# Kernel tuning notes

Hardware: AMD Instinct MI355X
Metric: run time of the kernel (lower is better)

Reference implementation:

```python
import jax, jax.numpy as jnp
import numpy as np

H = 64  # hidden_size, hard-coded in module


def _lstm_layer(xs, W_ih, W_hh, b_ih, b_hh):
    """Run one LSTM layer over time-major xs [T, B, D_in].
    PyTorch gate order: i, f, g, o. Returns (hs [T,B,H], h_last [B,H])."""
    T, B, _ = xs.shape
    b = b_ih + b_hh
    # Precompute input contribution for all timesteps: [T, B, 4H]
    x_gates = jnp.einsum('tbd,gd->tbg', xs, W_ih) + b

    def step(carry, xg_t):
        h, c = carry
        gates = xg_t + h @ W_hh.T  # [B, 4H]
        i, f, g, o = jnp.split(gates, 4, axis=-1)
        i = jax.nn.sigmoid(i)
        f = jax.nn.sigmoid(f)
        g = jnp.tanh(g)
        o = jax.nn.sigmoid(o)
        c = f * c + i * g
        h = o * jnp.tanh(c)
        return (h, c), h

    h0 = jnp.zeros((B, H), xs.dtype)
    c0 = jnp.zeros((B, H), xs.dtype)
    (h_last, _), hs = jax.lax.scan(step, (h0, c0), x_gates)
    return hs, h_last


def setup_inputs() -> dict:
    key = jax.random.key(0)
    ks = jax.random.split(key, 12)
    B, T, C_in, E = 256, 4000, 1, 128
    s0 = 1.0 / np.sqrt(H)  # PyTorch LSTM init scale
    inp = {
        'x': jax.random.normal(ks[0], (B, T, C_in), jnp.float32),
        'W_ih0': jax.random.uniform(ks[1], (4 * H, C_in), jnp.float32, -s0, s0),
        'W_hh0': jax.random.uniform(ks[2], (4 * H, H), jnp.float32, -s0, s0),
        'b_ih0': jax.random.uniform(ks[3], (4 * H,), jnp.float32, -s0, s0),
        'b_hh0': jax.random.uniform(ks[4], (4 * H,), jnp.float32, -s0, s0),
        'W_ih1': jax.random.uniform(ks[5], (4 * H, H), jnp.float32, -s0, s0),
        'W_hh1': jax.random.uniform(ks[6], (4 * H, H), jnp.float32, -s0, s0),
        'b_ih1': jax.random.uniform(ks[7], (4 * H,), jnp.float32, -s0, s0),
        'b_hh1': jax.random.uniform(ks[8], (4 * H,), jnp.float32, -s0, s0),
        'W_fc': jax.random.uniform(ks[9], (E, H), jnp.float32, -s0, s0),
        'b_fc': jax.random.uniform(ks[10], (E,), jnp.float32, -s0, s0),
    }
    return inp


def reference(x, W_ih0, W_hh0, b_ih0, b_hh0, W_ih1, W_hh1, b_ih1, b_hh1, W_fc, b_fc):
    # x: [B, T, 1] (batch_first) -> time-major [T, B, 1]
    xs = jnp.swapaxes(x.astype(jnp.float32), 0, 1)
    hs0, _ = _lstm_layer(xs, W_ih0, W_hh0, b_ih0, b_hh0)
    _, h_last = _lstm_layer(hs0, W_ih1, W_hh1, b_ih1, b_hh1)
    # fc on final hidden state of the last layer: [B, E]
    return h_last @ W_fc.T + b_fc
```

## Files before the change

kernel.cpp:

```cpp
#include <hip/hip_runtime.h>

#define TT 4000
#define HH 64
#define NB 256
#define EE 128

typedef __attribute__((ext_vector_type(2))) _Float16 h2;
typedef __attribute__((ext_vector_type(8))) _Float16 h8;

__device__ __forceinline__ float ftanh(float x) {
    return fmaf(2.f, __builtin_amdgcn_rcpf(1.f + __expf(-2.f * x)), -1.f);
}

#if __has_builtin(__builtin_amdgcn_fdot2)
#define FDOT2(a, b, c) __builtin_amdgcn_fdot2((a), (b), (c), false)
#else
#define FDOT2(a, b, c) fmaf((float)(a).x, (float)(b).x, fmaf((float)(a).y, (float)(b).y, (c)))
#endif

#define H2V(V, i) (__builtin_shufflevector((V), (V), 2 * (i), 2 * (i) + 1))

template <int CTRL>
__device__ __forceinline__ float dpp_mov(float v) {
    return __int_as_float(__builtin_amdgcn_update_dpp(
        0, __float_as_int(v), CTRL, 0xF, 0xF, true));
}
#define DPP_XOR1 0xB1
#define DPP_XOR2 0x4E
#define DPP_FB   0x44
#define DPP_OB   0xEE
#define DPP_SHR4 0x114

#define CVT2(d0, d1, s) h2 d0 = h2{(_Float16)(s).x, (_Float16)(s).y}, \
                           d1 = h2{(_Float16)(s).z, (_Float16)(s).w};

__global__ __launch_bounds__(512, 2)
void lstm2_fc_kernel(const float* __restrict__ x,
                     const float* __restrict__ W_ih0,
                     const float* __restrict__ W_hh0,
                     const float* __restrict__ b_ih0,
                     const float* __restrict__ b_hh0,
                     const float* __restrict__ W_ih1,
                     const float* __restrict__ W_hh1,
                     const float* __restrict__ b_ih1,
                     const float* __restrict__ b_hh1,
                     const float* __restrict__ W_fc,
                     const float* __restrict__ b_fc,
                     float* __restrict__ out)
{
    const int b    = blockIdx.x;
    const int tid  = threadIdx.x;
    const int w    = tid >> 6;
    const int lane = tid & 63;
    const int ss   = lane & 1;
    const int uu   = (lane >> 1) & 1;
    const int pp   = (lane >> 2) & 1;
    const int nn   = (lane >> 3) & 1;
    const int n    = w * 8 + (lane >> 4) * 2 + nn;
    const int gidx = pp + 2 * uu;

    __shared__ float x_s[TT];
    __shared__ __align__(16) _Float16 hbuf[2][2 * HH];

    for (int t = tid; t < TT; t += 512) x_s[t] = x[(size_t)b * TT + t];
    if (tid < 4 * HH) ((_Float16*)hbuf)[tid] = (_Float16)0.f;

    const int row = gidx * HH + n;
    const float4* p0 = (const float4*)(W_hh0 + row * HH + ss * 32);
    const float4* p1 = (const float4*)(W_ih1 + row * HH + ss * 32);
    const float4* p2 = (const float4*)(W_hh1 + row * HH + ss * 32);
    float4 a0 = p0[0], a1 = p0[1], a2 = p0[2], a3 = p0[3];
    float4 a4 = p0[4], a5 = p0[5], a6 = p0[6], a7 = p0[7];
    float4 e0 = p1[0], e1 = p1[1], e2 = p1[2], e3 = p1[3];
    float4 e4 = p1[4], e5 = p1[5], e6 = p1[6], e7 = p1[7];
    float4 d0 = p2[0], d1 = p2[1], d2 = p2[2], d3 = p2[3];
    float4 d4 = p2[4], d5 = p2[5], d6 = p2[6], d7 = p2[7];
    CVT2(A0,  A1,  a0) CVT2(A2,  A3,  a1) CVT2(A4,  A5,  a2) CVT2(A6,  A7,  a3)
    CVT2(A8,  A9,  a4) CVT2(A10, A11, a5) CVT2(A12, A13, a6) CVT2(A14, A15, a7)
    CVT2(B0,  B1,  e0) CVT2(B2,  B3,  e1) CVT2(B4,  B5,  e2) CVT2(B6,  B7,  e3)
    CVT2(B8,  B9,  e4) CVT2(B10, B11, e5) CVT2(B12, B13, e6) CVT2(B14, B15, e7)
    CVT2(C0,  C1,  d0) CVT2(C2,  C3,  d1) CVT2(C4,  C5,  d2) CVT2(C6,  C7,  d3)
    CVT2(C8,  C9,  d4) CVT2(C10, C11, d5) CVT2(C12, C13, d6) CVT2(C14, C15, d7)

    float wx  = W_ih0[row];
    float bb0 = b_ih0[row] + b_hh0[row];
    float bb1 = b_ih1[row] + b_hh1[row];

    asm volatile("" : "+v"(A0), "+v"(A1), "+v"(A2),  "+v"(A3),
                      "+v"(A4), "+v"(A5), "+v"(A6),  "+v"(A7),
                      "+v"(A8), "+v"(A9), "+v"(A10), "+v"(A11),
                      "+v"(A12),"+v"(A13),"+v"(A14), "+v"(A15),
                      "+v"(B0), "+v"(B1), "+v"(B2),  "+v"(B3),
                      "+v"(B4), "+v"(B5), "+v"(B6),  "+v"(B7));
    asm volatile("" : "+v"(B8), "+v"(B9), "+v"(B10), "+v"(B11),
                      "+v"(B12),"+v"(B13),"+v"(B14), "+v"(B15),
                      "+v"(C0), "+v"(C1), "+v"(C2),  "+v"(C3),
                      "+v"(C4), "+v"(C5), "+v"(C6),  "+v"(C7),
                      "+v"(C8), "+v"(C9), "+v"(C10), "+v"(C11),
                      "+v"(C12),"+v"(C13),"+v"(C14), "+v"(C15),
                      "+v"(wx), "+v"(bb0),"+v"(bb1));

    const bool isg = (gidx == 2);
    const float kk = isg ? -2.f : -1.f;
    const float mm = isg ?  2.f :  1.f;
    const float aa = isg ? -1.f :  0.f;

    const bool wlane = (pp == 1) && (uu == 0);
    const int  hoff  = ss * HH + n;
    float cc = 0.f;

    __syncthreads();

    for (int t = 0; t <= TT; ++t) {
        const float xt = x_s[(t < TT) ? t : 0];
        const h8* hb = (const h8*)hbuf[t & 1];
        h8 Ha = hb[4 * ss + 0], Hc = hb[4 * ss + 1];
        h8 He = hb[4 * ss + 2], Hg = hb[4 * ss + 3];
        h8 Ga = hb[8 + 4 * ss + 0], Gc = hb[8 + 4 * ss + 1];
        h8 Ge = hb[8 + 4 * ss + 2], Gg = hb[8 + 4 * ss + 3];

        float acc0 = ss ? 0.f : fmaf(xt, wx, bb0);
        float acc1 = ss ? 0.f : bb1;
        acc0 = FDOT2(A0,  H2V(Ha, 0), acc0); acc0 = FDOT2(A1,  H2V(Ha, 1), acc0);
        acc0 = FDOT2(A2,  H2V(Ha, 2), acc0); acc0 = FDOT2(A3,  H2V(Ha, 3), acc0);
        acc0 = FDOT2(A4,  H2V(Hc, 0), acc0); acc0 = FDOT2(A5,  H2V(Hc, 1), acc0);
        acc0 = FDOT2(A6,  H2V(Hc, 2), acc0); acc0 = FDOT2(A7,  H2V(Hc, 3), acc0);
        acc0 = FDOT2(A8,  H2V(He, 0), acc0); acc0 = FDOT2(A9,  H2V(He, 1), acc0);
        acc0 = FDOT2(A10, H2V(He, 2), acc0); acc0 = FDOT2(A11, H2V(He, 3), acc0);
        acc0 = FDOT2(A12, H2V(Hg, 0), acc0); acc0 = FDOT2(A13, H2V(Hg, 1), acc0);
        acc0 = FDOT2(A14, H2V(Hg, 2), acc0); acc0 = FDOT2(A15, H2V(Hg, 3), acc0);

        acc1 = FDOT2(B0,  H2V(Ha, 0), acc1); acc1 = FDOT2(B1,  H2V(Ha, 1), acc1);
        acc1 = FDOT2(B2,  H2V(Ha, 2), acc1); acc1 = FDOT2(B3,  H2V(Ha, 3), acc1);
        acc1 = FDOT2(B4,  H2V(Hc, 0), acc1); acc1 = FDOT2(B5,  H2V(Hc, 1), acc1);
        acc1 = FDOT2(B6,  H2V(Hc, 2), acc1); acc1 = FDOT2(B7,  H2V(Hc, 3), acc1);
        acc1 = FDOT2(B8,  H2V(He, 0), acc1); acc1 = FDOT2(B9,  H2V(He, 1), acc1);
        acc1 = FDOT2(B10, H2V(He, 2), acc1); acc1 = FDOT2(B11, H2V(He, 3), acc1);
        acc1 = FDOT2(B12, H2V(Hg, 0), acc1); acc1 = FDOT2(B13, H2V(Hg, 1), acc1);
        acc1 = FDOT2(B14, H2V(Hg, 2), acc1); acc1 = FDOT2(B15, H2V(Hg, 3), acc1);
        acc1 = FDOT2(C0,  H2V(Ga, 0), acc1); acc1 = FDOT2(C1,  H2V(Ga, 1), acc1);
        acc1 = FDOT2(C2,  H2V(Ga, 2), acc1); acc1 = FDOT2(C3,  H2V(Ga, 3), acc1);
        acc1 = FDOT2(C4,  H2V(Gc, 0), acc1); acc1 = FDOT2(C5,  H2V(Gc, 1), acc1);
        acc1 = FDOT2(C6,  H2V(Gc, 2), acc1); acc1 = FDOT2(C7,  H2V(Gc, 3), acc1);
        acc1 = FDOT2(C8,  H2V(Ge, 0), acc1); acc1 = FDOT2(C9,  H2V(Ge, 1), acc1);
        acc1 = FDOT2(C10, H2V(Ge, 2), acc1); acc1 = FDOT2(C11, H2V(Ge, 3), acc1);
        acc1 = FDOT2(C12, H2V(Gg, 0), acc1); acc1 = FDOT2(C13, H2V(Gg, 1), acc1);
        acc1 = FDOT2(C14, H2V(Gg, 2), acc1); acc1 = FDOT2(C15, H2V(Gg, 3), acc1);

        acc0 += dpp_mov<DPP_XOR1>(acc0);
        acc1 += dpp_mov<DPP_XOR1>(acc1);

        float z  = ss ? acc1 : acc0;
        float ez = __expf(kk * z);
        float val = fmaf(mm, __builtin_amdgcn_rcpf(1.f + ez), aa);

        float igq = val * dpp_mov<DPP_XOR2>(val);
        float ig  = dpp_mov<DPP_SHR4>(igq);
        float fb  = dpp_mov<DPP_FB>(val);
        float ob  = dpp_mov<DPP_OB>(val);

        float cn = fmaf(fb, cc, ig);
        float hn = ob * ftanh(cn);
        bool ok = ss ? (t > 0) : (t < TT);
        cc = ok ? cn : cc;
        if (wlane && ok) hbuf[(t + 1) & 1][hoff] = (_Float16)hn;

        __syncthreads();
    }

    if (tid < EE) {
        const _Float16* h1f = &hbuf[(TT + 1) & 1][HH];
        float acc = b_fc[tid];
        const float4* wf = (const float4*)(W_fc + tid * HH);
        #pragma unroll
        for (int k = 0; k < HH / 4; ++k) {
            float4 v = wf[k];
            acc = fmaf(v.x, (float)h1f[4*k+0], acc);
            acc = fmaf(v.y, (float)h1f[4*k+1], acc);
            acc = fmaf(v.z, (float)h1f[4*k+2], acc);
            acc = fmaf(v.w, (float)h1f[4*k+3], acc);
        }
        out[(size_t)b * EE + tid] = acc;
    }
}

extern "C" void kernel_launch(void* const* d_in, const int* in_sizes, int n_in,
                              void* d_out, int out_size, void* d_ws, size_t ws_size,
                              hipStream_t stream) {
    const float* x     = (const float*)d_in[0];
    const float* W_ih0 = (const float*)d_in[1];
    const float* W_hh0 = (const float*)d_in[2];
    const float* b_ih0 = (const float*)d_in[3];
    const float* b_hh0 = (const float*)d_in[4];
    const float* W_ih1 = (const float*)d_in[5];
    const float* W_hh1 = (const float*)d_in[6];
    const float* b_ih1 = (const float*)d_in[7];
    const float* b_hh1 = (const float*)d_in[8];
    const float* W_fc  = (const float*)d_in[9];
    const float* b_fc  = (const float*)d_in[10];
    float* out = (float*)d_out;

    lstm2_fc_kernel<<<dim3(NB), dim3(512), 0, stream>>>(
        x, W_ih0, W_hh0, b_ih0, b_hh0, W_ih1, W_hh1, b_ih1, b_hh1, W_fc, b_fc, out);
}
```

Baseline: 1.960 ms.

## Halve block size and have each thread compute two hidden units

```diff
diff --git a/kernel.cpp b/kernel.cpp
--- a/kernel.cpp
+++ b/kernel.cpp
@@ -34,7 +34,13 @@
 #define CVT2(d0, d1, s) h2 d0 = h2{(_Float16)(s).x, (_Float16)(s).y}, \
                            d1 = h2{(_Float16)(s).z, (_Float16)(s).w};
 
-__global__ __launch_bounds__(512, 2)
+#define D4(acc, W0, W1, W2, W3, Hv) \
+    acc = FDOT2(W0, H2V(Hv, 0), acc); \
+    acc = FDOT2(W1, H2V(Hv, 1), acc); \
+    acc = FDOT2(W2, H2V(Hv, 2), acc); \
+    acc = FDOT2(W3, H2V(Hv, 3), acc);
+
+__global__ __launch_bounds__(256, 1)
 void lstm2_fc_kernel(const float* __restrict__ x,
                      const float* __restrict__ W_ih0,
                      const float* __restrict__ W_hh0,
@@ -56,35 +62,55 @@
     const int uu   = (lane >> 1) & 1;
     const int pp   = (lane >> 2) & 1;
     const int nn   = (lane >> 3) & 1;
-    const int n    = w * 8 + (lane >> 4) * 2 + nn;
+    const int na   = w * 8 + (lane >> 4) * 2 + nn;
+    const int nb   = na + 32;
     const int gidx = pp + 2 * uu;
 
     __shared__ float x_s[TT];
     __shared__ __align__(16) _Float16 hbuf[2][2 * HH];
 
-    for (int t = tid; t < TT; t += 512) x_s[t] = x[(size_t)b * TT + t];
+    for (int t = tid; t < TT; t += 256) x_s[t] = x[(size_t)b * TT + t];
     if (tid < 4 * HH) ((_Float16*)hbuf)[tid] = (_Float16)0.f;
 
-    const int row = gidx * HH + n;
-    const float4* p0 = (const float4*)(W_hh0 + row * HH + ss * 32);
-    const float4* p1 = (const float4*)(W_ih1 + row * HH + ss * 32);
-    const float4* p2 = (const float4*)(W_hh1 + row * HH + ss * 32);
-    float4 a0 = p0[0], a1 = p0[1], a2 = p0[2], a3 = p0[3];
-    float4 a4 = p0[4], a5 = p0[5], a6 = p0[6], a7 = p0[7];
-    float4 e0 = p1[0], e1 = p1[1], e2 = p1[2], e3 = p1[3];
-    float4 e4 = p1[4], e5 = p1[5], e6 = p1[6], e7 = p1[7];
-    float4 d0 = p2[0], d1 = p2[1], d2 = p2[2], d3 = p2[3];
-    float4 d4 = p2[4], d5 = p2[5], d6 = p2[6], d7 = p2[7];
-    CVT2(A0,  A1,  a0) CVT2(A2,  A3,  a1) CVT2(A4,  A5,  a2) CVT2(A6,  A7,  a3)
-    CVT2(A8,  A9,  a4) CVT2(A10, A11, a5) CVT2(A12, A13, a6) CVT2(A14, A15, a7)
-    CVT2(B0,  B1,  e0) CVT2(B2,  B3,  e1) CVT2(B4,  B5,  e2) CVT2(B6,  B7,  e3)
-    CVT2(B8,  B9,  e4) CVT2(B10, B11, e5) CVT2(B12, B13, e6) CVT2(B14, B15, e7)
-    CVT2(C0,  C1,  d0) CVT2(C2,  C3,  d1) CVT2(C4,  C5,  d2) CVT2(C6,  C7,  d3)
-    CVT2(C8,  C9,  d4) CVT2(C10, C11, d5) CVT2(C12, C13, d6) CVT2(C14, C15, d7)
-
-    float wx  = W_ih0[row];
-    float bb0 = b_ih0[row] + b_hh0[row];
-    float bb1 = b_ih1[row] + b_hh1[row];
+    const int rowa = gidx * HH + na;
+    const int rowb = gidx * HH + nb;
+    const float4* p0 = (const float4*)(W_hh0 + rowa * HH + ss * 32);
+    const float4* p1 = (const float4*)(W_ih1 + rowa * HH + ss * 32);
+    const float4* p2 = (const float4*)(W_hh1 + rowa * HH + ss * 32);
+    const float4* p3 = (const float4*)(W_hh0 + rowb * HH + ss * 32);
+    const float4* p4 = (const float4*)(W_ih1 + rowb * HH + ss * 32);
+    const float4* p5 = (const float4*)(W_hh1 + rowb * HH + ss * 32);
+    float4 qa0 = p0[0], qa1 = p0[1], qa2 = p0[2], qa3 = p0[3];
+    float4 qa4 = p0[4], qa5 = p0[5], qa6 = p0[6], qa7 = p0[7];
+    float4 qb0 = p1[0], qb1 = p1[1], qb2 = p1[2], qb3 = p1[3];
+    float4 qb4 = p1[4], qb5 = p1[5], qb6 = p1[6], qb7 = p1[7];
+    float4 qc0 = p2[0], qc1 = p2[1], qc2 = p2[2], qc3 = p2[3];
+    float4 qc4 = p2[4], qc5 = p2[5], qc6 = p2[6], qc7 = p2[7];
+    float4 qd0 = p3[0], qd1 = p3[1], qd2 = p3[2], qd3 = p3[3];
+    float4 qd4 = p3[4], qd5 = p3[5], qd6 = p3[6], qd7 = p3[7];
+    float4 qe0 = p4[0], qe1 = p4[1], qe2 = p4[2], qe3 = p4[3];
+    float4 qe4 = p4[4], qe5 = p4[5], qe6 = p4[6], qe7 = p4[7];
+    float4 qf0 = p5[0], qf1 = p5[1], qf2 = p5[2], qf3 = p5[3];
+    float4 qf4 = p5[4], qf5 = p5[5], qf6 = p5[6], qf7 = p5[7];
+    CVT2(A0,  A1,  qa0) CVT2(A2,  A3,  qa1) CVT2(A4,  A5,  qa2) CVT2(A6,  A7,  qa3)
+    CVT2(A8,  A9,  qa4) CVT2(A10, A11, qa5) CVT2(A12, A13, qa6) CVT2(A14, A15, qa7)
+    CVT2(B0,  B1,  qb0) CVT2(B2,  B3,  qb1) CVT2(B4,  B5,  qb2) CVT2(B6,  B7,  qb3)
+    CVT2(B8,  B9,  qb4) CVT2(B10, B11, qb5) CVT2(B12, B13, qb6) CVT2(B14, B15, qb7)
+    CVT2(C0,  C1,  qc0) CVT2(C2,  C3,  qc1) CVT2(C4,  C5,  qc2) CVT2(C6,  C7,  qc3)
+    CVT2(C8,  C9,  qc4) CVT2(C10, C11, qc5) CVT2(C12, C13, qc6) CVT2(C14, C15, qc7)
+    CVT2(D0,  D1,  qd0) CVT2(D2,  D3,  qd1) CVT2(D4,  D5,  qd2) CVT2(D6,  D7,  qd3)
+    CVT2(D8,  D9,  qd4) CVT2(D10, D11, qd5) CVT2(D12, D13, qd6) CVT2(D14, D15, qd7)
+    CVT2(E0,  E1,  qe0) CVT2(E2,  E3,  qe1) CVT2(E4,  E5,  qe2) CVT2(E6,  E7,  qe3)
+    CVT2(E8,  E9,  qe4) CVT2(E10, E11, qe5) CVT2(E12, E13, qe6) CVT2(E14, E15, qe7)
+    CVT2(F0,  F1,  qf0) CVT2(F2,  F3,  qf1) CVT2(F4,  F5,  qf2) CVT2(F6,  F7,  qf3)
+    CVT2(F8,  F9,  qf4) CVT2(F10, F11, qf5) CVT2(F12, F13, qf6) CVT2(F14, F15, qf7)
+
+    float wxa  = W_ih0[rowa];
+    float wxb  = W_ih0[rowb];
+    float bb0a = b_ih0[rowa] + b_hh0[rowa];
+    float bb0b = b_ih0[rowb] + b_hh0[rowb];
+    float bb1a = b_ih1[rowa] + b_hh1[rowa];
+    float bb1b = b_ih1[rowb] + b_hh1[rowb];
 
     asm volatile("" : "+v"(A0), "+v"(A1), "+v"(A2),  "+v"(A3),
                       "+v"(A4), "+v"(A5), "+v"(A6),  "+v"(A7),
@@ -97,8 +123,21 @@
                       "+v"(C0), "+v"(C1), "+v"(C2),  "+v"(C3),
                       "+v"(C4), "+v"(C5), "+v"(C6),  "+v"(C7),
                       "+v"(C8), "+v"(C9), "+v"(C10), "+v"(C11),
-                      "+v"(C12),"+v"(C13),"+v"(C14), "+v"(C15),
-                      "+v"(wx), "+v"(bb0),"+v"(bb1));
+                      "+v"(C12),"+v"(C13),"+v"(C14), "+v"(C15));
+    asm volatile("" : "+v"(D0), "+v"(D1), "+v"(D2),  "+v"(D3),
+                      "+v"(D4), "+v"(D5), "+v"(D6),  "+v"(D7),
+                      "+v"(D8), "+v"(D9), "+v"(D10), "+v"(D11),
+                      "+v"(D12),"+v"(D13),"+v"(D14), "+v"(D15),
+                      "+v"(E0), "+v"(E1), "+v"(E2),  "+v"(E3),
+                      "+v"(E4), "+v"(E5), "+v"(E6),  "+v"(E7));
+    asm volatile("" : "+v"(E8), "+v"(E9), "+v"(E10), "+v"(E11),
+                      "+v"(E12),"+v"(E13),"+v"(E14), "+v"(E15),
+                      "+v"(F0), "+v"(F1), "+v"(F2),  "+v"(F3),
+                      "+v"(F4), "+v"(F5), "+v"(F6),  "+v"(F7),
+                      "+v"(F8), "+v"(F9), "+v"(F10), "+v"(F11),
+                      "+v"(F12),"+v"(F13),"+v"(F14), "+v"(F15));
+    asm volatile("" : "+v"(wxa), "+v"(wxb), "+v"(bb0a),
+                      "+v"(bb0b),"+v"(bb1a),"+v"(bb1b));
 
     const bool isg = (gidx == 2);
     const float kk = isg ? -2.f : -1.f;
@@ -106,8 +145,9 @@
     const float aa = isg ? -1.f :  0.f;
 
     const bool wlane = (pp == 1) && (uu == 0);
-    const int  hoff  = ss * HH + n;
-    float cc = 0.f;
+    const int  hoffa = ss * HH + na;
+    const int  hoffb = ss * HH + nb;
+    float cca = 0.f, ccb = 0.f;
 
     __syncthreads();
 
@@ -119,51 +159,57 @@
         h8 Ga = hb[8 + 4 * ss + 0], Gc = hb[8 + 4 * ss + 1];
         h8 Ge = hb[8 + 4 * ss + 2], Gg = hb[8 + 4 * ss + 3];
 
-        float acc0 = ss ? 0.f : fmaf(xt, wx, bb0);
-        float acc1 = ss ? 0.f : bb1;
-        acc0 = FDOT2(A0,  H2V(Ha, 0), acc0); acc0 = FDOT2(A1,  H2V(Ha, 1), acc0);
-        acc0 = FDOT2(A2,  H2V(Ha, 2), acc0); acc0 = FDOT2(A3,  H2V(Ha, 3), acc0);
-        acc0 = FDOT2(A4,  H2V(Hc, 0), acc0); acc0 = FDOT2(A5,  H2V(Hc, 1), acc0);
-        acc0 = FDOT2(A6,  H2V(Hc, 2), acc0); acc0 = FDOT2(A7,  H2V(Hc, 3), acc0);
-        acc0 = FDOT2(A8,  H2V(He, 0), acc0); acc0 = FDOT2(A9,  H2V(He, 1), acc0);
-        acc0 = FDOT2(A10, H2V(He, 2), acc0); acc0 = FDOT2(A11, H2V(He, 3), acc0);
-        acc0 = FDOT2(A12, H2V(Hg, 0), acc0); acc0 = FDOT2(A13, H2V(Hg, 1), acc0);
-        acc0 = FDOT2(A14, H2V(Hg, 2), acc0); acc0 = FDOT2(A15, H2V(Hg, 3), acc0);
-
-        acc1 = FDOT2(B0,  H2V(Ha, 0), acc1); acc1 = FDOT2(B1,  H2V(Ha, 1), acc1);
-        acc1 = FDOT2(B2,  H2V(Ha, 2), acc1); acc1 = FDOT2(B3,  H2V(Ha, 3), acc1);
-        acc1 = FDOT2(B4,  H2V(Hc, 0), acc1); acc1 = FDOT2(B5,  H2V(Hc, 1), acc1);
-        acc1 = FDOT2(B6,  H2V(Hc, 2), acc1); acc1 = FDOT2(B7,  H2V(Hc, 3), acc1);
-        acc1 = FDOT2(B8,  H2V(He, 0), acc1); acc1 = FDOT2(B9,  H2V(He, 1), acc1);
-        acc1 = FDOT2(B10, H2V(He, 2), acc1); acc1 = FDOT2(B11, H2V(He, 3), acc1);
-        acc1 = FDOT2(B12, H2V(Hg, 0), acc1); acc1 = FDOT2(B13, H2V(Hg, 1), acc1);
-        acc1 = FDOT2(B14, H2V(Hg, 2), acc1); acc1 = FDOT2(B15, H2V(Hg, 3), acc1);
-        acc1 = FDOT2(C0,  H2V(Ga, 0), acc1); acc1 = FDOT2(C1,  H2V(Ga, 1), acc1);
-        acc1 = FDOT2(C2,  H2V(Ga, 2), acc1); acc1 = FDOT2(C3,  H2V(Ga, 3), acc1);
-        acc1 = FDOT2(C4,  H2V(Gc, 0), acc1); acc1 = FDOT2(C5,  H2V(Gc, 1), acc1);
-        acc1 = FDOT2(C6,  H2V(Gc, 2), acc1); acc1 = FDOT2(C7,  H2V(Gc, 3), acc1);
-        acc1 = FDOT2(C8,  H2V(Ge, 0), acc1); acc1 = FDOT2(C9,  H2V(Ge, 1), acc1);
-        acc1 = FDOT2(C10, H2V(Ge, 2), acc1); acc1 = FDOT2(C11, H2V(Ge, 3), acc1);
-        acc1 = FDOT2(C12, H2V(Gg, 0), acc1); acc1 = FDOT2(C13, H2V(Gg, 1), acc1);
-        acc1 = FDOT2(C14, H2V(Gg, 2), acc1); acc1 = FDOT2(C15, H2V(Gg, 3), acc1);
-
-        acc0 += dpp_mov<DPP_XOR1>(acc0);
-        acc1 += dpp_mov<DPP_XOR1>(acc1);
-
-        float z  = ss ? acc1 : acc0;
-        float ez = __expf(kk * z);
-        float val = fmaf(mm, __builtin_amdgcn_rcpf(1.f + ez), aa);
-
-        float igq = val * dpp_mov<DPP_XOR2>(val);
-        float ig  = dpp_mov<DPP_SHR4>(igq);
-        float fb  = dpp_mov<DPP_FB>(val);
-        float ob  = dpp_mov<DPP_OB>(val);
-
-        float cn = fmaf(fb, cc, ig);
-        float hn = ob * ftanh(cn);
+        float acc0a = ss ? 0.f : fmaf(xt, wxa, bb0a);
+        float acc0b = ss ? 0.f : fmaf(xt, wxb, bb0b);
+        float acc1a = ss ? 0.f : bb1a;
+        float acc1b = ss ? 0.f : bb1b;
+
+        D4(acc0a, A0,  A1,  A2,  A3,  Ha)  D4(acc0b, D0,  D1,  D2,  D3,  Ha)
+        D4(acc1a, B0,  B1,  B2,  B3,  Ha)  D4(acc1b, E0,  E1,  E2,  E3,  Ha)
+        D4(acc0a, A4,  A5,  A6,  A7,  Hc)  D4(acc0b, D4,  D5,  D6,  D7,  Hc)
+        D4(acc1a, B4,  B5,  B6,  B7,  Hc)  D4(acc1b, E4,  E5,  E6,  E7,  Hc)
+        D4(acc0a, A8,  A9,  A10, A11, He)  D4(acc0b, D8,  D9,  D10, D11, He)
+        D4(acc1a, B8,  B9,  B10, B11, He)  D4(acc1b, E8,  E9,  E10, E11, He)
+        D4(acc0a, A12, A13, A14, A15, Hg)  D4(acc0b, D12, D13, D14, D15, Hg)
+        D4(acc1a, B12, B13, B14, B15, Hg)  D4(acc1b, E12, E13, E14, E15, Hg)
+        D4(acc1a, C0,  C1,  C2,  C3,  Ga)  D4(acc1b, F0,  F1,  F2,  F3,  Ga)
+        D4(acc1a, C4,  C5,  C6,  C7,  Gc)  D4(acc1b, F4,  F5,  F6,  F7,  Gc)
+        D4(acc1a, C8,  C9,  C10, C11, Ge)  D4(acc1b, F8,  F9,  F10, F11, Ge)
+        D4(acc1a, C12, C13, C14, C15, Gg)  D4(acc1b, F12, F13, F14, F15, Gg)
+
+        acc0a += dpp_mov<DPP_XOR1>(acc0a);
+        acc0b += dpp_mov<DPP_XOR1>(acc0b);
+        acc1a += dpp_mov<DPP_XOR1>(acc1a);
+        acc1b += dpp_mov<DPP_XOR1>(acc1b);
+
+        float za  = ss ? acc1a : acc0a;
+        float zb  = ss ? acc1b : acc0b;
+        float eza = __expf(kk * za);
+        float ezb = __expf(kk * zb);
+        float va  = fmaf(mm, __builtin_amdgcn_rcpf(1.f + eza), aa);
+        float vb  = fmaf(mm, __builtin_amdgcn_rcpf(1.f + ezb), aa);
+
+        float igqa = va * dpp_mov<DPP_XOR2>(va);
+        float igqb = vb * dpp_mov<DPP_XOR2>(vb);
+        float iga  = dpp_mov<DPP_SHR4>(igqa);
+        float igb  = dpp_mov<DPP_SHR4>(igqb);
+        float fba  = dpp_mov<DPP_FB>(va);
+        float fbb  = dpp_mov<DPP_FB>(vb);
+        float oba  = dpp_mov<DPP_OB>(va);
+        float obb  = dpp_mov<DPP_OB>(vb);
+
+        float cna = fmaf(fba, cca, iga);
+        float cnb = fmaf(fbb, ccb, igb);
+        float hna = oba * ftanh(cna);
+        float hnb = obb * ftanh(cnb);
         bool ok = ss ? (t > 0) : (t < TT);
-        cc = ok ? cn : cc;
-        if (wlane && ok) hbuf[(t + 1) & 1][hoff] = (_Float16)hn;
+        cca = ok ? cna : cca;
+        ccb = ok ? cnb : ccb;
+        if (wlane && ok) {
+            _Float16* hw = hbuf[(t + 1) & 1];
+            hw[hoffa] = (_Float16)hna;
+            hw[hoffb] = (_Float16)hnb;
+        }
 
         __syncthreads();
     }
@@ -200,6 +246,6 @@
     const float* b_fc  = (const float*)d_in[10];
     float* out = (float*)d_out;
 
-    lstm2_fc_kernel<<<dim3(NB), dim3(512), 0, stream>>>(
+    lstm2_fc_kernel<<<dim3(NB), dim3(256), 0, stream>>>(
         x, W_ih0, W_hh0, b_ih0, b_hh0, W_ih1, W_hh1, b_ih1, b_hh1, W_fc, b_fc, out);
 }
```

Result: faster. 1.821 ms (-7.1%).

## Use MFMA 16x16x32 f16 for recurrent gate matvecs with 256-thread blocks

Applied to the files above, without the earlier changes.

```diff
diff --git a/kernel.cpp b/kernel.cpp
--- a/kernel.cpp
+++ b/kernel.cpp
@@ -5,36 +5,25 @@
 #define NB 256
 #define EE 128
 
-typedef __attribute__((ext_vector_type(2))) _Float16 h2;
 typedef __attribute__((ext_vector_type(8))) _Float16 h8;
+typedef __attribute__((ext_vector_type(4))) float f4;
 
 __device__ __forceinline__ float ftanh(float x) {
     return fmaf(2.f, __builtin_amdgcn_rcpf(1.f + __expf(-2.f * x)), -1.f);
 }
+__device__ __forceinline__ float fsig(float x) {
+    return __builtin_amdgcn_rcpf(1.f + __expf(-x));
+}
 
-#if __has_builtin(__builtin_amdgcn_fdot2)
-#define FDOT2(a, b, c) __builtin_amdgcn_fdot2((a), (b), (c), false)
-#else
-#define FDOT2(a, b, c) fmaf((float)(a).x, (float)(b).x, fmaf((float)(a).y, (float)(b).y, (c)))
-#endif
+#define MF(A, B, C) __builtin_amdgcn_mfma_f32_16x16x32_f16((A), (B), (C), 0, 0, 0)
 
-#define H2V(V, i) (__builtin_shufflevector((V), (V), 2 * (i), 2 * (i) + 1))
+__device__ __forceinline__ h8 ld8h(const float* p) {
+    f4 a = ((const f4*)p)[0], c = ((const f4*)p)[1];
+    return h8{(_Float16)a.x, (_Float16)a.y, (_Float16)a.z, (_Float16)a.w,
+              (_Float16)c.x, (_Float16)c.y, (_Float16)c.z, (_Float16)c.w};
+}
 
-template <int CTRL>
-__device__ __forceinline__ float dpp_mov(float v) {
-    return __int_as_float(__builtin_amdgcn_update_dpp(
-        0, __float_as_int(v), CTRL, 0xF, 0xF, true));
-}
-#define DPP_XOR1 0xB1
-#define DPP_XOR2 0x4E
-#define DPP_FB   0x44
-#define DPP_OB   0xEE
-#define DPP_SHR4 0x114
-
-#define CVT2(d0, d1, s) h2 d0 = h2{(_Float16)(s).x, (_Float16)(s).y}, \
-                           d1 = h2{(_Float16)(s).z, (_Float16)(s).w};
-
-__global__ __launch_bounds__(512, 2)
+__global__ __launch_bounds__(256, 1)
 void lstm2_fc_kernel(const float* __restrict__ x,
                      const float* __restrict__ W_ih0,
                      const float* __restrict__ W_hh0,
@@ -52,118 +41,95 @@
     const int tid  = threadIdx.x;
     const int w    = tid >> 6;
     const int lane = tid & 63;
-    const int ss   = lane & 1;
-    const int uu   = (lane >> 1) & 1;
-    const int pp   = (lane >> 2) & 1;
-    const int nn   = (lane >> 3) & 1;
-    const int n    = w * 8 + (lane >> 4) * 2 + nn;
-    const int gidx = pp + 2 * uu;
+    const int cidx = lane & 15;
+    const int kgrp = lane >> 4;
+    const int n    = w * 16 + cidx;
+    const bool act = (kgrp == 0);
 
     __shared__ float x_s[TT];
     __shared__ __align__(16) _Float16 hbuf[2][2 * HH];
 
-    for (int t = tid; t < TT; t += 512) x_s[t] = x[(size_t)b * TT + t];
+    for (int t = tid; t < TT; t += 256) x_s[t] = x[(size_t)b * TT + t];
     if (tid < 4 * HH) ((_Float16*)hbuf)[tid] = (_Float16)0.f;
 
-    const int row = gidx * HH + n;
-    const float4* p0 = (const float4*)(W_hh0 + row * HH + ss * 32);
-    const float4* p1 = (const float4*)(W_ih1 + row * HH + ss * 32);
-    const float4* p2 = (const float4*)(W_hh1 + row * HH + ss * 32);
-    float4 a0 = p0[0], a1 = p0[1], a2 = p0[2], a3 = p0[3];
-    float4 a4 = p0[4], a5 = p0[5], a6 = p0[6], a7 = p0[7];
-    float4 e0 = p1[0], e1 = p1[1], e2 = p1[2], e3 = p1[3];
-    float4 e4 = p1[4], e5 = p1[5], e6 = p1[6], e7 = p1[7];
-    float4 d0 = p2[0], d1 = p2[1], d2 = p2[2], d3 = p2[3];
-    float4 d4 = p2[4], d5 = p2[5], d6 = p2[6], d7 = p2[7];
-    CVT2(A0,  A1,  a0) CVT2(A2,  A3,  a1) CVT2(A4,  A5,  a2) CVT2(A6,  A7,  a3)
-    CVT2(A8,  A9,  a4) CVT2(A10, A11, a5) CVT2(A12, A13, a6) CVT2(A14, A15, a7)
-    CVT2(B0,  B1,  e0) CVT2(B2,  B3,  e1) CVT2(B4,  B5,  e2) CVT2(B6,  B7,  e3)
-    CVT2(B8,  B9,  e4) CVT2(B10, B11, e5) CVT2(B12, B13, e6) CVT2(B14, B15, e7)
-    CVT2(C0,  C1,  d0) CVT2(C2,  C3,  d1) CVT2(C4,  C5,  d2) CVT2(C6,  C7,  d3)
-    CVT2(C8,  C9,  d4) CVT2(C10, C11, d5) CVT2(C12, C13, d6) CVT2(C14, C15, d7)
+    const int rI = 0 * HH + n, rF = 1 * HH + n, rG = 2 * HH + n, rO = 3 * HH + n;
+    const int kb0 = kgrp * 8, kb1 = 32 + kgrp * 8;
 
-    float wx  = W_ih0[row];
-    float bb0 = b_ih0[row] + b_hh0[row];
-    float bb1 = b_ih1[row] + b_hh1[row];
+    h8 BI0a = ld8h(W_hh0 + rI * HH + kb0), BI0b = ld8h(W_hh0 + rI * HH + kb1);
+    h8 BF0a = ld8h(W_hh0 + rF * HH + kb0), BF0b = ld8h(W_hh0 + rF * HH + kb1);
+    h8 BG0a = ld8h(W_hh0 + rG * HH + kb0), BG0b = ld8h(W_hh0 + rG * HH + kb1);
+    h8 BO0a = ld8h(W_hh0 + rO * HH + kb0), BO0b = ld8h(W_hh0 + rO * HH + kb1);
+    h8 BI1a = ld8h(W_ih1 + rI * HH + kb0), BI1b = ld8h(W_ih1 + rI * HH + kb1);
+    h8 BF1a = ld8h(W_ih1 + rF * HH + kb0), BF1b = ld8h(W_ih1 + rF * HH + kb1);
+    h8 BG1a = ld8h(W_ih1 + rG * HH + kb0), BG1b = ld8h(W_ih1 + rG * HH + kb1);
+    h8 BO1a = ld8h(W_ih1 + rO * HH + kb0), BO1b = ld8h(W_ih1 + rO * HH + kb1);
+    h8 BI1c = ld8h(W_hh1 + rI * HH + kb0), BI1d = ld8h(W_hh1 + rI * HH + kb1);
+    h8 BF1c = ld8h(W_hh1 + rF * HH + kb0), BF1d = ld8h(W_hh1 + rF * HH + kb1);
+    h8 BG1c = ld8h(W_hh1 + rG * HH + kb0), BG1d = ld8h(W_hh1 + rG * HH + kb1);
+    h8 BO1c = ld8h(W_hh1 + rO * HH + kb0), BO1d = ld8h(W_hh1 + rO * HH + kb1);
 
-    asm volatile("" : "+v"(A0), "+v"(A1), "+v"(A2),  "+v"(A3),
-                      "+v"(A4), "+v"(A5), "+v"(A6),  "+v"(A7),
-                      "+v"(A8), "+v"(A9), "+v"(A10), "+v"(A11),
-                      "+v"(A12),"+v"(A13),"+v"(A14), "+v"(A15),
-                      "+v"(B0), "+v"(B1), "+v"(B2),  "+v"(B3),
-                      "+v"(B4), "+v"(B5), "+v"(B6),  "+v"(B7));
-    asm volatile("" : "+v"(B8), "+v"(B9), "+v"(B10), "+v"(B11),
-                      "+v"(B12),"+v"(B13),"+v"(B14), "+v"(B15),
-                      "+v"(C0), "+v"(C1), "+v"(C2),  "+v"(C3),
-                      "+v"(C4), "+v"(C5), "+v"(C6),  "+v"(C7),
-                      "+v"(C8), "+v"(C9), "+v"(C10), "+v"(C11),
-                      "+v"(C12),"+v"(C13),"+v"(C14), "+v"(C15),
-                      "+v"(wx), "+v"(bb0),"+v"(bb1));
+    float wxI = W_ih0[rI], wxF = W_ih0[rF], wxG = W_ih0[rG], wxO = W_ih0[rO];
+    float bI0 = b_ih0[rI] + b_hh0[rI], bF0 = b_ih0[rF] + b_hh0[rF];
+    float bG0 = b_ih0[rG] + b_hh0[rG], bO0 = b_ih0[rO] + b_hh0[rO];
+    float bI1 = b_ih1[rI] + b_hh1[rI], bF1 = b_ih1[rF] + b_hh1[rF];
+    float bG1 = b_ih1[rG] + b_hh1[rG], bO1 = b_ih1[rO] + b_hh1[rO];
 
-    const bool isg = (gidx == 2);
-    const float kk = isg ? -2.f : -1.f;
-    const float mm = isg ?  2.f :  1.f;
-    const float aa = isg ? -1.f :  0.f;
+    asm volatile("" : "+v"(BI0a), "+v"(BI0b), "+v"(BF0a), "+v"(BF0b),
+                      "+v"(BG0a), "+v"(BG0b), "+v"(BO0a), "+v"(BO0b),
+                      "+v"(BI1a), "+v"(BI1b), "+v"(BF1a), "+v"(BF1b));
+    asm volatile("" : "+v"(BG1a), "+v"(BG1b), "+v"(BO1a), "+v"(BO1b),
+                      "+v"(BI1c), "+v"(BI1d), "+v"(BF1c), "+v"(BF1d),
+                      "+v"(BG1c), "+v"(BG1d), "+v"(BO1c), "+v"(BO1d));
+    asm volatile("" : "+v"(wxI), "+v"(wxF), "+v"(wxG), "+v"(wxO),
+                      "+v"(bI0), "+v"(bF0), "+v"(bG0), "+v"(bO0),
+                      "+v"(bI1), "+v"(bF1), "+v"(bG1), "+v"(bO1));
 
-    const bool wlane = (pp == 1) && (uu == 0);
-    const int  hoff  = ss * HH + n;
-    float cc = 0.f;
+    float cc0 = 0.f, cc1 = 0.f;
 
     __syncthreads();
 
     for (int t = 0; t <= TT; ++t) {
         const float xt = x_s[(t < TT) ? t : 0];
         const h8* hb = (const h8*)hbuf[t & 1];
-        h8 Ha = hb[4 * ss + 0], Hc = hb[4 * ss + 1];
-        h8 He = hb[4 * ss + 2], Hg = hb[4 * ss + 3];
-        h8 Ga = hb[8 + 4 * ss + 0], Gc = hb[8 + 4 * ss + 1];
-        h8 Ge = hb[8 + 4 * ss + 2], Gg = hb[8 + 4 * ss + 3];
+        h8 A0a = hb[kgrp],     A0b = hb[4 + kgrp];
+        h8 A1a = hb[8 + kgrp], A1b = hb[12 + kgrp];
 
-        float acc0 = ss ? 0.f : fmaf(xt, wx, bb0);
-        float acc1 = ss ? 0.f : bb1;
-        acc0 = FDOT2(A0,  H2V(Ha, 0), acc0); acc0 = FDOT2(A1,  H2V(Ha, 1), acc0);
-        acc0 = FDOT2(A2,  H2V(Ha, 2), acc0); acc0 = FDOT2(A3,  H2V(Ha, 3), acc0);
-        acc0 = FDOT2(A4,  H2V(Hc, 0), acc0); acc0 = FDOT2(A5,  H2V(Hc, 1), acc0);
-        acc0 = FDOT2(A6,  H2V(Hc, 2), acc0); acc0 = FDOT2(A7,  H2V(Hc, 3), acc0);
-        acc0 = FDOT2(A8,  H2V(He, 0), acc0); acc0 = FDOT2(A9,  H2V(He, 1), acc0);
-        acc0 = FDOT2(A10, H2V(He, 2), acc0); acc0 = FDOT2(A11, H2V(He, 3), acc0);
-        acc0 = FDOT2(A12, H2V(Hg, 0), acc0); acc0 = FDOT2(A13, H2V(Hg, 1), acc0);
-        acc0 = FDOT2(A14, H2V(Hg, 2), acc0); acc0 = FDOT2(A15, H2V(Hg, 3), acc0);
+        f4 aI0 = {act ? fmaf(xt, wxI, bI0) : 0.f, 0.f, 0.f, 0.f};
+        f4 aF0 = {act ? fmaf(xt, wxF, bF0) : 0.f, 0.f, 0.f, 0.f};
+        f4 aG0 = {act ? fmaf(xt, wxG, bG0) : 0.f, 0.f, 0.f, 0.f};
+        f4 aO0 = {act ? fmaf(xt, wxO, bO0) : 0.f, 0.f, 0.f, 0.f};
+        f4 aI1 = {act ? bI1 : 0.f, 0.f, 0.f, 0.f};
+        f4 aF1 = {act ? bF1 : 0.f, 0.f, 0.f, 0.f};
+        f4 aG1 = {act ? bG1 : 0.f, 0.f, 0.f, 0.f};
+        f4 aO1 = {act ? bO1 : 0.f, 0.f, 0.f, 0.f};
 
-        acc1 = FDOT2(B0,  H2V(Ha, 0), acc1); acc1 = FDOT2(B1,  H2V(Ha, 1), acc1);
-        acc1 = FDOT2(B2,  H2V(Ha, 2), acc1); acc1 = FDOT2(B3,  H2V(Ha, 3), acc1);
-        acc1 = FDOT2(B4,  H2V(Hc, 0), acc1); acc1 = FDOT2(B5,  H2V(Hc, 1), acc1);
-        acc1 = FDOT2(B6,  H2V(Hc, 2), acc1); acc1 = FDOT2(B7,  H2V(Hc, 3), acc1);
-        acc1 = FDOT2(B8,  H2V(He, 0), acc1); acc1 = FDOT2(B9,  H2V(He, 1), acc1);
-        acc1 = FDOT2(B10, H2V(He, 2), acc1); acc1 = FDOT2(B11, H2V(He, 3), acc1);
-        acc1 = FDOT2(B12, H2V(Hg, 0), acc1); acc1 = FDOT2(B13, H2V(Hg, 1), acc1);
-        acc1 = FDOT2(B14, H2V(Hg, 2), acc1); acc1 = FDOT2(B15, H2V(Hg, 3), acc1);
-        acc1 = FDOT2(C0,  H2V(Ga, 0), acc1); acc1 = FDOT2(C1,  H2V(Ga, 1), acc1);
-        acc1 = FDOT2(C2,  H2V(Ga, 2), acc1); acc1 = FDOT2(C3,  H2V(Ga, 3), acc1);
-        acc1 = FDOT2(C4,  H2V(Gc, 0), acc1); acc1 = FDOT2(C5,  H2V(Gc, 1), acc1);
-        acc1 = FDOT2(C6,  H2V(Gc, 2), acc1); acc1 = FDOT2(C7,  H2V(Gc, 3), acc1);
-        acc1 = FDOT2(C8,  H2V(Ge, 0), acc1); acc1 = FDOT2(C9,  H2V(Ge, 1), acc1);
-        acc1 = FDOT2(C10, H2V(Ge, 2), acc1); acc1 = FDOT2(C11, H2V(Ge, 3), acc1);
-        acc1 = FDOT2(C12, H2V(Gg, 0), acc1); acc1 = FDOT2(C13, H2V(Gg, 1), acc1);
-        acc1 = FDOT2(C14, H2V(Gg, 2), acc1); acc1 = FDOT2(C15, H2V(Gg, 3), acc1);
+        aI0 = MF(A0a, BI0a, aI0); aF0 = MF(A0a, BF0a, aF0);
+        aG0 = MF(A0a, BG0a, aG0); aO0 = MF(A0a, BO0a, aO0);
+        aI0 = MF(A0b, BI0b, aI0); aF0 = MF(A0b, BF0b, aF0);
+        aG0 = MF(A0b, BG0b, aG0); aO0 = MF(A0b, BO0b, aO0);
+        aI1 = MF(A0a, BI1a, aI1); aF1 = MF(A0a, BF1a, aF1);
+        aG1 = MF(A0a, BG1a, aG1); aO1 = MF(A0a, BO1a, aO1);
+        aI1 = MF(A0b, BI1b, aI1); aF1 = MF(A0b, BF1b, aF1);
+        aG1 = MF(A0b, BG1b, aG1); aO1 = MF(A0b, BO1b, aO1);
+        aI1 = MF(A1a, BI1c, aI1); aF1 = MF(A1a, BF1c, aF1);
+        aG1 = MF(A1a, BG1c, aG1); aO1 = MF(A1a, BO1c, aO1);
+        aI1 = MF(A1b, BI1d, aI1); aF1 = MF(A1b, BF1d, aF1);
+        aG1 = MF(A1b, BG1d, aG1); aO1 = MF(A1b, BO1d, aO1);
 
-        acc0 += dpp_mov<DPP_XOR1>(acc0);
-        acc1 += dpp_mov<DPP_XOR1>(acc1);
-
-        float z  = ss ? acc1 : acc0;
-        float ez = __expf(kk * z);
-        float val = fmaf(mm, __builtin_amdgcn_rcpf(1.f + ez), aa);
-
-        float igq = val * dpp_mov<DPP_XOR2>(val);
-        float ig  = dpp_mov<DPP_SHR4>(igq);
-        float fb  = dpp_mov<DPP_FB>(val);
-        float ob  = dpp_mov<DPP_OB>(val);
-
-        float cn = fmaf(fb, cc, ig);
-        float hn = ob * ftanh(cn);
-        bool ok = ss ? (t > 0) : (t < TT);
-        cc = ok ? cn : cc;
-        if (wlane && ok) hbuf[(t + 1) & 1][hoff] = (_Float16)hn;
+        float i0 = fsig(aI0.x), f0v = fsig(aF0.x);
+        float g0 = ftanh(aG0.x), o0 = fsig(aO0.x);
+        float i1 = fsig(aI1.x), f1v = fsig(aF1.x);
+        float g1 = ftanh(aG1.x), o1 = fsig(aO1.x);
+        float nc0 = fmaf(f0v, cc0, i0 * g0);
+        float nc1 = fmaf(f1v, cc1, i1 * g1);
+        const bool ok0 = (t < TT), ok1 = (t > 0);
+        cc0 = ok0 ? nc0 : cc0;
+        cc1 = ok1 ? nc1 : cc1;
+        float h0n = o0 * ftanh(nc0);
+        float h1n = o1 * ftanh(nc1);
+        _Float16* hw = hbuf[(t + 1) & 1];
+        if (act && ok0) hw[n] = (_Float16)h0n;
+        if (act && ok1) hw[HH + n] = (_Float16)h1n;
 
         __syncthreads();
     }
@@ -200,6 +166,6 @@
     const float* b_fc  = (const float*)d_in[10];
     float* out = (float*)d_out;
 
-    lstm2_fc_kernel<<<dim3(NB), dim3(512), 0, stream>>>(
+    lstm2_fc_kernel<<<dim3(NB), dim3(256), 0, stream>>>(
         x, W_ih0, W_hh0, b_ih0, b_hh0, W_ih1, W_hh1, b_ih1, b_hh1, W_fc, b_fc, out);
 }
```

Result: slower. 2.082 ms (+6.2%).
